# Kernel tuning notes

Measured on AMD Instinct MI355X. Metric: run time of the kernel, lower is better.

## Reference

```python
import jax, jax.numpy as jnp
import numpy as np

DIM = 1024
NUM_HEADS = 16
HEAD_DIM = DIM // NUM_HEADS
SCALE = HEAD_DIM ** -0.5


def setup_inputs() -> dict:
    key = jax.random.key(0)
    ks = jax.random.split(key, 8)
    B, N, L = 2, 256, 8192
    x = jax.random.normal(ks[0], (B, N, DIM), dtype=jnp.float32)
    past_k = jax.random.normal(ks[1], (B, NUM_HEADS, L, HEAD_DIM), dtype=jnp.float32)
    past_v = jax.random.normal(ks[2], (B, NUM_HEADS, L, HEAD_DIM), dtype=jnp.float32)
    s = DIM ** -0.5
    w_qkv = jax.random.normal(ks[3], (DIM, 3 * DIM), dtype=jnp.float32) * s
    b_qkv = jnp.zeros((3 * DIM,), dtype=jnp.float32)
    w_proj = jax.random.normal(ks[4], (DIM, DIM), dtype=jnp.float32) * s
    b_proj = jnp.zeros((DIM,), dtype=jnp.float32)
    return {"x": x, "past_k": past_k, "past_v": past_v,
            "w_qkv": w_qkv, "b_qkv": b_qkv, "w_proj": w_proj, "b_proj": b_proj}


def reference(x, past_k, past_v, w_qkv, b_qkv, w_proj, b_proj):
    B, N, C = x.shape
    qkv = (x @ w_qkv + b_qkv).reshape(B, N, 3, NUM_HEADS, HEAD_DIM)
    qkv = jnp.transpose(qkv, (2, 0, 3, 1, 4))
    q, k_new, v_new = qkv[0], qkv[1], qkv[2]
    # Streaming KV cache append (torch.cat along seq dim)
    k_all = jnp.concatenate([past_k, k_new], axis=-2)  # [B, H, L+N, D]
    v_all = jnp.concatenate([past_v, v_new], axis=-2)
    # Scaled dot-product attention (non-causal full attention over cache)
    scores = jnp.einsum("bhnd,bhld->bhnl", q, k_all) * SCALE
    attn = jax.nn.softmax(scores, axis=-1)
    out = jnp.einsum("bhnl,bhld->bhnd", attn, v_all)  # [B, H, N, D]
    out = jnp.transpose(out, (0, 2, 1, 3)).reshape(B, N, C)
    return out @ w_proj + b_proj
```

## Files before the change

kernel.cpp:

```cpp
#include <hip/hip_runtime.h>
#include <hip/hip_bf16.h>


#define BB 2
#define NH 16
#define NQ 256
#define HD 64
#define DIMC 1024
#define LPAST 8192
#define TOTK 8448
#define NSPLIT 16

typedef __attribute__((ext_vector_type(8))) short short8;
typedef __attribute__((ext_vector_type(4))) float f32x4;
typedef __attribute__((ext_vector_type(16))) float f32x16;
typedef __attribute__((ext_vector_type(4))) int int4v;

#define DEVI static __device__ __forceinline__

DEVI float exp2g(float x) { return __builtin_amdgcn_exp2f(x); }

DEVI int cvtpk(float lo, float hi) {
  int r;
  asm("v_cvt_pk_bf16_f32 %0, %1, %2" : "=v"(r) : "v"(lo), "v"(hi));
  return r;
}
DEVI short f2bf(float f) {
  union { float f; unsigned u; } v; v.f = f;
  unsigned r = v.u + 0x7FFFu + ((v.u >> 16) & 1u);
  return (short)(r >> 16);
}
DEVI void ldsbar() {
  asm volatile("s_waitcnt lgkmcnt(0)" ::: "memory");
  __builtin_amdgcn_s_barrier();
}

template<int MODE>
__global__ __launch_bounds__(256, 2) void gemm_k(
    const float* __restrict__ A, const float* __restrict__ Bm,
    const float* __restrict__ bias, float* __restrict__ Cout,
    short* __restrict__ qbuf, float* __restrict__ knew, float* __restrict__ vnew,
    int M, int Nn, int K)
{
  __shared__ alignas(16) short As[64][72];
  __shared__ alignas(16) short Bs[64][72];
  const int tid = threadIdx.x;
  const int lane = tid & 63, wave = tid >> 6;
  const int nblk = Nn >> 6;
  const int bi = blockIdx.x / nblk, bj = blockIdx.x % nblk;
  const int wm = wave >> 1, wn = wave & 1;
  const int g = lane >> 4, l16 = lane & 15;
  f32x4 acc[2][2] = {};
  const int r = tid >> 2, q4 = (tid & 3) << 4;

  for (int k0 = 0; k0 < K; k0 += 64) {
    const float* pa = A + (size_t)(bi * 64 + r) * K + (k0 + q4);
    float4 a0 = ((const float4*)pa)[0];
    float4 a1 = ((const float4*)pa)[1];
    float4 a2 = ((const float4*)pa)[2];
    float4 a3 = ((const float4*)pa)[3];
    const float* pb = Bm + (size_t)(k0 + r) * Nn + (bj * 64 + q4);
    float4 b0 = ((const float4*)pb)[0];
    float4 b1 = ((const float4*)pb)[1];
    float4 b2 = ((const float4*)pb)[2];
    float4 b3 = ((const float4*)pb)[3];
    ldsbar();
    {
      int4v p0 = {cvtpk(a0.x,a0.y), cvtpk(a0.z,a0.w), cvtpk(a1.x,a1.y), cvtpk(a1.z,a1.w)};
      int4v p1 = {cvtpk(a2.x,a2.y), cvtpk(a2.z,a2.w), cvtpk(a3.x,a3.y), cvtpk(a3.z,a3.w)};
      *(int4v*)&As[r][q4]     = p0;
      *(int4v*)&As[r][q4 + 8] = p1;
    }
    Bs[q4+ 0][r] = f2bf(b0.x); Bs[q4+ 1][r] = f2bf(b0.y);
    Bs[q4+ 2][r] = f2bf(b0.z); Bs[q4+ 3][r] = f2bf(b0.w);
    Bs[q4+ 4][r] = f2bf(b1.x); Bs[q4+ 5][r] = f2bf(b1.y);
    Bs[q4+ 6][r] = f2bf(b1.z); Bs[q4+ 7][r] = f2bf(b1.w);
    Bs[q4+ 8][r] = f2bf(b2.x); Bs[q4+ 9][r] = f2bf(b2.y);
    Bs[q4+10][r] = f2bf(b2.z); Bs[q4+11][r] = f2bf(b2.w);
    Bs[q4+12][r] = f2bf(b3.x); Bs[q4+13][r] = f2bf(b3.y);
    Bs[q4+14][r] = f2bf(b3.z); Bs[q4+15][r] = f2bf(b3.w);
    ldsbar();
    #pragma unroll
    for (int kf = 0; kf < 2; ++kf) {
      short8 af[2], bfv[2];
      #pragma unroll
      for (int mt = 0; mt < 2; ++mt)
        af[mt] = *(const short8*)&As[wm*32 + mt*16 + l16][kf*32 + g*8];
      #pragma unroll
      for (int nt = 0; nt < 2; ++nt)
        bfv[nt] = *(const short8*)&Bs[wn*32 + nt*16 + l16][kf*32 + g*8];
      #pragma unroll
      for (int mt = 0; mt < 2; ++mt)
        #pragma unroll
        for (int nt = 0; nt < 2; ++nt)
          acc[mt][nt] = __builtin_amdgcn_mfma_f32_16x16x32_bf16(
              af[mt], bfv[nt], acc[mt][nt], 0, 0, 0);
    }
  }

  #pragma unroll
  for (int mt = 0; mt < 2; ++mt)
    #pragma unroll
    for (int nt = 0; nt < 2; ++nt)
      #pragma unroll
      for (int rg = 0; rg < 4; ++rg) {
        int row = bi*64 + wm*32 + mt*16 + g*4 + rg;
        int col = bj*64 + wn*32 + nt*16 + l16;
        float val = acc[mt][nt][rg] + bias[col];
        if (MODE == 0) {
          Cout[(size_t)row * Nn + col] = val;
        } else {
          int which = col >> 10, cc = col & 1023;
          int h = cc >> 6, d = cc & 63;
          int b = row >> 8, n = row & 255;
          size_t idx = (((size_t)(b*NH + h))*NQ + n)*HD + d;
          if (which == 0)      qbuf[idx] = f2bf(val * 0.180336878f);
          else if (which == 1) knew[idx] = val;
          else                 vnew[idx] = val;
        }
      }
}

__global__ __launch_bounds__(256, 2) void attn_k(
    const short* __restrict__ qbuf, const float* __restrict__ pastk,
    const float* __restrict__ pastv, const float* __restrict__ knew,
    const float* __restrict__ vnew, _Float16* __restrict__ opart,
    float* __restrict__ mbuf, float* __restrict__ lbuf)
{
  __shared__ alignas(16) short Kt[2][64][64];
  __shared__ alignas(16) short Vt[3][64][64];
  const int tid = threadIdx.x;
  const int lane = tid & 63, qg = tid >> 6;
  const int h = lane >> 5, c = lane & 31;
  const int s = blockIdx.x & (NSPLIT - 1), bh = blockIdx.x / NSPLIT;
  const int kr = tid >> 2, kd16 = (tid & 3) << 4;
  const int vq2 = tid & 31, dg = tid >> 5;
  const int key0 = 2 * vq2;
  const int vpi = ((key0>>5)<<5) | (((key0>>3)&1)<<4) | (((key0>>2)&1)<<3)
                | (((key0>>4)&1)<<2) | (key0&3);
  const int csw = (c & 7) << 3;

  short8 qfA[4], qfB[4];
  #pragma unroll
  for (int dk = 0; dk < 4; ++dk) {
    qfA[dk] = *(const short8*)(qbuf + ((size_t)bh*NQ + qg*64 + c)*HD + 16*dk + 8*h);
    qfB[dk] = *(const short8*)(qbuf + ((size_t)bh*NQ + qg*64 + 32 + c)*HD + 16*dk + 8*h);
  }

  f32x16 accA[2] = {}, accB[2] = {};
  float mA = -INFINITY, lA = 0.f, mB = -INFINITY, lB = 0.f;
  short8 paA[4], paB[4];

  const int first  = 8*s + (s < 4 ? s : 4);
  const int nsteps = 8 + (s < 4 ? 1 : 0);

  float kst[16], vAr[8], vBr[8];
  auto load = [&](int step) {
    const float* kp = (step < 128)
        ? pastk + ((size_t)bh*LPAST + step*64 + kr)*HD + kd16
        : knew  + ((size_t)bh*NQ + (step - 128)*64 + kr)*HD + kd16;
    *(float4*)&kst[0]  = ((const float4*)kp)[0];
    *(float4*)&kst[4]  = ((const float4*)kp)[1];
    *(float4*)&kst[8]  = ((const float4*)kp)[2];
    *(float4*)&kst[12] = ((const float4*)kp)[3];
    const float* vq = (step < 128)
        ? pastv + ((size_t)bh*LPAST + step*64 + key0)*HD + 8*dg
        : vnew  + ((size_t)bh*NQ + (step - 128)*64 + key0)*HD + 8*dg;
    *(float4*)&vAr[0] = ((const float4*)vq)[0];
    *(float4*)&vAr[4] = ((const float4*)vq)[1];
    *(float4*)&vBr[0] = ((const float4*)(vq + HD))[0];
    *(float4*)&vBr[4] = ((const float4*)(vq + HD))[1];
  };
  auto stage_for = [&](int it2) {
    int kb = it2 & 1, vb = it2 % 3;
    int4v k0 = {cvtpk(kst[0],kst[1]),  cvtpk(kst[2],kst[3]),
                cvtpk(kst[4],kst[5]),  cvtpk(kst[6],kst[7])};
    int4v k1 = {cvtpk(kst[8],kst[9]),  cvtpk(kst[10],kst[11]),
                cvtpk(kst[12],kst[13]), cvtpk(kst[14],kst[15])};
    *(int4v*)&Kt[kb][kr][kd16 ^ ((kr & 7) << 3)]       = k0;
    *(int4v*)&Kt[kb][kr][(kd16 + 8) ^ ((kr & 7) << 3)] = k1;
    #pragma unroll
    for (int i = 0; i < 8; ++i) {
      int row = 8*dg + i;
      *(int*)&Vt[vb][row][vpi ^ (i << 3)] = cvtpk(vAr[i], vBr[i]);
    }
  };

  load(first);
  stage_for(0);
  if (nsteps > 1) load(first + 1);
  ldsbar();

  for (int it = 0; it < nsteps; ++it) {
    const int kb = it & 1;

    f32x16 svA0 = {}, svA1 = {}, svB0 = {}, svB1 = {};
    __builtin_amdgcn_s_setprio(1);
    if (it > 0) {
      const int pvb = (it - 1) % 3;
      #pragma unroll
      for (int kc = 0; kc < 4; ++kc) {
        #pragma unroll
        for (int dt = 0; dt < 2; ++dt) {
          short8 vf = *(const short8*)&Vt[pvb][32*dt + c][(16*kc + 8*h) ^ csw];
          accA[dt] = __builtin_amdgcn_mfma_f32_32x32x16_bf16(paA[kc], vf, accA[dt], 0,0,0);
          accB[dt] = __builtin_amdgcn_mfma_f32_32x32x16_bf16(paB[kc], vf, accB[dt], 0,0,0);
        }
      }
    }
    #pragma unroll
    for (int dk = 0; dk < 4; ++dk) {
      short8 k0 = *(const short8*)&Kt[kb][c][(16*dk + 8*h) ^ csw];
      svA0 = __builtin_amdgcn_mfma_f32_32x32x16_bf16(k0, qfA[dk], svA0, 0,0,0);
      svB0 = __builtin_amdgcn_mfma_f32_32x32x16_bf16(k0, qfB[dk], svB0, 0,0,0);
    }
    #pragma unroll
    for (int dk = 0; dk < 4; ++dk) {
      short8 k1 = *(const short8*)&Kt[kb][32 + c][(16*dk + 8*h) ^ csw];
      svA1 = __builtin_amdgcn_mfma_f32_32x32x16_bf16(k1, qfA[dk], svA1, 0,0,0);
      svB1 = __builtin_amdgcn_mfma_f32_32x32x16_bf16(k1, qfB[dk], svB1, 0,0,0);
    }
    __builtin_amdgcn_s_setprio(0);

    if (it + 1 < nsteps) {
      stage_for(it + 1);
      if (it + 2 < nsteps) load(first + it + 2);
    }

    {
      float t16[16];
      #pragma unroll
      for (int r = 0; r < 16; ++r) t16[r] = fmaxf(svA0[r], svA1[r]);
      #pragma unroll
      for (int w = 8; w >= 1; w >>= 1)
        #pragma unroll
        for (int r = 0; r < w; ++r) t16[r] = fmaxf(t16[r], t16[r + w]);
      if (!__all(t16[0] <= mA + 8.f)) {
        float mx = fmaxf(t16[0], __shfl_xor(t16[0], 32));
        float mn = fmaxf(mA, mx);
        float al = exp2g(mA - mn);
        lA *= al;
        #pragma unroll
        for (int r = 0; r < 16; ++r) {
          float a = __shfl(al, (r&3) + 8*(r>>2) + 4*h);
          accA[0][r] *= a; accA[1][r] *= a;
        }
        mA = mn;
      }
      float ss = 0.f;
      #pragma unroll
      for (int r = 0; r < 16; ++r) {
        float p0 = exp2g(svA0[r] - mA); svA0[r] = p0;
        float p1 = exp2g(svA1[r] - mA); svA1[r] = p1;
        ss += p0 + p1;
      }
      lA += ss;
      #pragma unroll
      for (int kc = 0; kc < 4; ++kc) {
        int4v w;
        #pragma unroll
        for (int jd = 0; jd < 4; ++jd) {
          int r0 = 8*(jd>>1) + 4*(kc&1) + 2*(jd&1);
          w[jd] = (kc < 2) ? cvtpk(svA0[r0], svA0[r0+1])
                           : cvtpk(svA1[r0], svA1[r0+1]);
        }
        paA[kc] = __builtin_bit_cast(short8, w);
      }
    }
    {
      float t16[16];
      #pragma unroll
      for (int r = 0; r < 16; ++r) t16[r] = fmaxf(svB0[r], svB1[r]);
      #pragma unroll
      for (int w = 8; w >= 1; w >>= 1)
        #pragma unroll
        for (int r = 0; r < w; ++r) t16[r] = fmaxf(t16[r], t16[r + w]);
      if (!__all(t16[0] <= mB + 8.f)) {
        float mx = fmaxf(t16[0], __shfl_xor(t16[0], 32));
        float mn = fmaxf(mB, mx);
        float al = exp2g(mB - mn);
        lB *= al;
        #pragma unroll
        for (int r = 0; r < 16; ++r) {
          float a = __shfl(al, (r&3) + 8*(r>>2) + 4*h);
          accB[0][r] *= a; accB[1][r] *= a;
        }
        mB = mn;
      }
      float ss = 0.f;
      #pragma unroll
      for (int r = 0; r < 16; ++r) {
        float p0 = exp2g(svB0[r] - mB); svB0[r] = p0;
        float p1 = exp2g(svB1[r] - mB); svB1[r] = p1;
        ss += p0 + p1;
      }
      lB += ss;
      #pragma unroll
      for (int kc = 0; kc < 4; ++kc) {
        int4v w;
        #pragma unroll
        for (int jd = 0; jd < 4; ++jd) {
          int r0 = 8*(jd>>1) + 4*(kc&1) + 2*(jd&1);
          w[jd] = (kc < 2) ? cvtpk(svB0[r0], svB0[r0+1])
                           : cvtpk(svB1[r0], svB1[r0+1]);
        }
        paB[kc] = __builtin_bit_cast(short8, w);
      }
    }

    if (it + 1 < nsteps) ldsbar();
  }

  {
    const int pvb = (nsteps - 1) % 3;
    #pragma unroll
    for (int kc = 0; kc < 4; ++kc) {
      #pragma unroll
      for (int dt = 0; dt < 2; ++dt) {
        short8 vf = *(const short8*)&Vt[pvb][32*dt + c][(16*kc + 8*h) ^ csw];
        accA[dt] = __builtin_amdgcn_mfma_f32_32x32x16_bf16(paA[kc], vf, accA[dt], 0,0,0);
        accB[dt] = __builtin_amdgcn_mfma_f32_32x32x16_bf16(paB[kc], vf, accB[dt], 0,0,0);
      }
    }
  }

  float lAt = lA + __shfl_xor(lA, 32);
  float lBt = lB + __shfl_xor(lB, 32);
  float rA = 1.0f / lAt, rB = 1.0f / lBt;
  size_t pbase = ((size_t)(bh * NSPLIT + s)) * NQ;
  #pragma unroll
  for (int r = 0; r < 16; ++r) {
    int rr = (r&3) + 8*(r>>2) + 4*h;
    float rAr = __shfl(rA, rr);
    float rBr = __shfl(rB, rr);
    #pragma unroll
    for (int dt = 0; dt < 2; ++dt) {
      opart[(pbase + qg*64 + rr)*HD + 32*dt + c]      = (_Float16)(accA[dt][r] * rAr);
      opart[(pbase + qg*64 + 32 + rr)*HD + 32*dt + c] = (_Float16)(accB[dt][r] * rBr);
    }
  }
  if (lane < 32) {
    mbuf[pbase + qg*64 + c]      = mA;
    lbuf[pbase + qg*64 + c]      = lAt;
    mbuf[pbase + qg*64 + 32 + c] = mB;
    lbuf[pbase + qg*64 + 32 + c] = lBt;
  }
}

__global__ __launch_bounds__(256) void combine_k(
    const _Float16* __restrict__ opart, const float* __restrict__ mbuf,
    const float* __restrict__ lbuf, float* __restrict__ attnout)
{
  const int lane = threadIdx.x & 63, wave = threadIdx.x >> 6;
  const int rid = blockIdx.x * 4 + wave;
  const int bh = rid >> 8, n = rid & 255;
  const int b = bh >> 4, h = bh & 15;
  float M = -INFINITY;
  float ms[NSPLIT], ls[NSPLIT];
  #pragma unroll
  for (int s = 0; s < NSPLIT; ++s) {
    size_t base = ((size_t)(bh * NSPLIT + s)) * NQ + n;
    ms[s] = mbuf[base]; ls[s] = lbuf[base];
    M = fmaxf(M, ms[s]);
  }
  float denom = 0.f, o = 0.f;
  #pragma unroll
  for (int s = 0; s < NSPLIT; ++s) {
    float w = exp2g(ms[s] - M) * ls[s];
    denom += w;
    o += w * (float)opart[(((size_t)(bh * NSPLIT + s)) * NQ + n) * HD + lane];
  }
  attnout[((size_t)(b * NQ + n)) * DIMC + h * HD + lane] = o / denom;
}

extern "C" void kernel_launch(void* const* d_in, const int* in_sizes, int n_in,
                              void* d_out, int out_size, void* d_ws, size_t ws_size,
                              hipStream_t stream)
{
  const float* x     = (const float*)d_in[0];
  const float* pastk = (const float*)d_in[1];
  const float* pastv = (const float*)d_in[2];
  const float* wqkv  = (const float*)d_in[3];
  const float* bqkv  = (const float*)d_in[4];
  const float* wproj = (const float*)d_in[5];
  const float* bproj = (const float*)d_in[6];
  float* out = (float*)d_out;
  char* ws = (char*)d_ws;

  size_t off = 0;
  short* qbuf     = (short*)(ws + off);     off += (size_t)BB*NH*NQ*HD*2;
  float* knew     = (float*)(ws + off);     off += (size_t)BB*NH*NQ*HD*4;
  float* vnew     = (float*)(ws + off);     off += (size_t)BB*NH*NQ*HD*4;
  _Float16* opart = (_Float16*)(ws + off);  off += (size_t)BB*NH*NSPLIT*NQ*HD*2;
  float* mbuf     = (float*)(ws + off);     off += (size_t)BB*NH*NSPLIT*NQ*4;
  float* lbuf     = (float*)(ws + off);     off += (size_t)BB*NH*NSPLIT*NQ*4;
  float* attnout  = (float*)(ws + off);     off += (size_t)BB*NQ*DIMC*4;

  gemm_k<1><<<(512/64)*(3072/64), 256, 0, stream>>>(
      x, wqkv, bqkv, nullptr, qbuf, knew, vnew, 512, 3072, 1024);
  attn_k<<<BB*NH*NSPLIT, 256, 0, stream>>>(
      qbuf, pastk, pastv, knew, vnew, opart, mbuf, lbuf);
  combine_k<<<BB*NH*NQ/4, 256, 0, stream>>>(opart, mbuf, lbuf, attnout);
  gemm_k<0><<<(512/64)*(1024/64), 256, 0, stream>>>(
      attnout, wproj, bproj, out, nullptr, nullptr, nullptr, 512, 1024, 1024);
}
```

Baseline: 84.53 us.

## Raise attention split count and occupancy, serialize QK halves to cut registers

Increases the KV split count from 16 to 24 and raises the launch bound to 3 blocks per CU, so more blocks are resident at once. To fit that register budget, the B-half score MFMAs now run after the A-half softmax instead of together with it, which shrinks the live score accumulators. The V load/staging pattern changes to four keys per thread with int2 LDS writes, and the split ranges are rebalanced for 132 steps over 24 splits. The cost is more partial results to merge and less overlap between the two query halves within a wave.

```diff
diff --git a/kernel.cpp b/kernel.cpp
--- a/kernel.cpp
+++ b/kernel.cpp
@@ -9,7 +9,7 @@
 #define DIMC 1024
 #define LPAST 8192
 #define TOTK 8448
-#define NSPLIT 16
+#define NSPLIT 24
 
 typedef __attribute__((ext_vector_type(8))) short short8;
 typedef __attribute__((ext_vector_type(4))) float f32x4;
@@ -121,7 +121,7 @@
       }
 }
 
-__global__ __launch_bounds__(256, 2) void attn_k(
+__global__ __launch_bounds__(256, 3) void attn_k(
     const short* __restrict__ qbuf, const float* __restrict__ pastk,
     const float* __restrict__ pastv, const float* __restrict__ knew,
     const float* __restrict__ vnew, _Float16* __restrict__ opart,
@@ -132,12 +132,12 @@
   const int tid = threadIdx.x;
   const int lane = tid & 63, qg = tid >> 6;
   const int h = lane >> 5, c = lane & 31;
-  const int s = blockIdx.x & (NSPLIT - 1), bh = blockIdx.x / NSPLIT;
+  const int s = blockIdx.x % NSPLIT, bh = blockIdx.x / NSPLIT;
   const int kr = tid >> 2, kd16 = (tid & 3) << 4;
-  const int vq2 = tid & 31, dg = tid >> 5;
-  const int key0 = 2 * vq2;
+  const int vq4 = tid & 15, dgg = tid >> 4;
+  const int key0 = 4 * vq4;
   const int vpi = ((key0>>5)<<5) | (((key0>>3)&1)<<4) | (((key0>>2)&1)<<3)
-                | (((key0>>4)&1)<<2) | (key0&3);
+                | (((key0>>4)&1)<<2);
   const int csw = (c & 7) << 3;
 
   short8 qfA[4], qfB[4];
@@ -151,10 +151,11 @@
   float mA = -INFINITY, lA = 0.f, mB = -INFINITY, lB = 0.f;
   short8 paA[4], paB[4];
 
-  const int first  = 8*s + (s < 4 ? s : 4);
-  const int nsteps = 8 + (s < 4 ? 1 : 0);
-
-  float kst[16], vAr[8], vBr[8];
+  const int first  = (s < 12) ? 6*s : 5*s + 12;
+  const int nsteps = (s < 12) ? 6 : 5;
+
+  float kst[16];
+  float4 vk0, vk1, vk2, vk3;
   auto load = [&](int step) {
     const float* kp = (step < 128)
         ? pastk + ((size_t)bh*LPAST + step*64 + kr)*HD + kd16
@@ -164,12 +165,12 @@
     *(float4*)&kst[8]  = ((const float4*)kp)[2];
     *(float4*)&kst[12] = ((const float4*)kp)[3];
     const float* vq = (step < 128)
-        ? pastv + ((size_t)bh*LPAST + step*64 + key0)*HD + 8*dg
-        : vnew  + ((size_t)bh*NQ + (step - 128)*64 + key0)*HD + 8*dg;
-    *(float4*)&vAr[0] = ((const float4*)vq)[0];
-    *(float4*)&vAr[4] = ((const float4*)vq)[1];
-    *(float4*)&vBr[0] = ((const float4*)(vq + HD))[0];
-    *(float4*)&vBr[4] = ((const float4*)(vq + HD))[1];
+        ? pastv + ((size_t)bh*LPAST + step*64 + key0)*HD + 4*dgg
+        : vnew  + ((size_t)bh*NQ + (step - 128)*64 + key0)*HD + 4*dgg;
+    vk0 = *(const float4*)(vq);
+    vk1 = *(const float4*)(vq + HD);
+    vk2 = *(const float4*)(vq + 2*HD);
+    vk3 = *(const float4*)(vq + 3*HD);
   };
   auto stage_for = [&](int it2) {
     int kb = it2 & 1, vb = it2 % 3;
@@ -179,10 +180,15 @@
                 cvtpk(kst[12],kst[13]), cvtpk(kst[14],kst[15])};
     *(int4v*)&Kt[kb][kr][kd16 ^ ((kr & 7) << 3)]       = k0;
     *(int4v*)&Kt[kb][kr][(kd16 + 8) ^ ((kr & 7) << 3)] = k1;
-    #pragma unroll
-    for (int i = 0; i < 8; ++i) {
-      int row = 8*dg + i;
-      *(int*)&Vt[vb][row][vpi ^ (i << 3)] = cvtpk(vAr[i], vBr[i]);
+    const float* f0 = (const float*)&vk0;
+    const float* f1 = (const float*)&vk1;
+    const float* f2 = (const float*)&vk2;
+    const float* f3 = (const float*)&vk3;
+    #pragma unroll
+    for (int i = 0; i < 4; ++i) {
+      int row = 4*dgg + i;
+      int2 w = make_int2(cvtpk(f0[i], f1[i]), cvtpk(f2[i], f3[i]));
+      *(int2*)&Vt[vb][row][vpi ^ ((row & 7) << 3)] = w;
     }
   };
 
@@ -194,7 +200,7 @@
   for (int it = 0; it < nsteps; ++it) {
     const int kb = it & 1;
 
-    f32x16 svA0 = {}, svA1 = {}, svB0 = {}, svB1 = {};
+    f32x16 svA0 = {}, svA1 = {};
     __builtin_amdgcn_s_setprio(1);
     if (it > 0) {
       const int pvb = (it - 1) % 3;
@@ -211,21 +217,11 @@
     #pragma unroll
     for (int dk = 0; dk < 4; ++dk) {
       short8 k0 = *(const short8*)&Kt[kb][c][(16*dk + 8*h) ^ csw];
+      short8 k1 = *(const short8*)&Kt[kb][32 + c][(16*dk + 8*h) ^ csw];
       svA0 = __builtin_amdgcn_mfma_f32_32x32x16_bf16(k0, qfA[dk], svA0, 0,0,0);
-      svB0 = __builtin_amdgcn_mfma_f32_32x32x16_bf16(k0, qfB[dk], svB0, 0,0,0);
-    }
-    #pragma unroll
-    for (int dk = 0; dk < 4; ++dk) {
-      short8 k1 = *(const short8*)&Kt[kb][32 + c][(16*dk + 8*h) ^ csw];
       svA1 = __builtin_amdgcn_mfma_f32_32x32x16_bf16(k1, qfA[dk], svA1, 0,0,0);
-      svB1 = __builtin_amdgcn_mfma_f32_32x32x16_bf16(k1, qfB[dk], svB1, 0,0,0);
     }
     __builtin_amdgcn_s_setprio(0);
-
-    if (it + 1 < nsteps) {
-      stage_for(it + 1);
-      if (it + 2 < nsteps) load(first + it + 2);
-    }
 
     {
       float t16[16];
@@ -267,6 +263,23 @@
         paA[kc] = __builtin_bit_cast(short8, w);
       }
     }
+
+    f32x16 svB0 = {}, svB1 = {};
+    __builtin_amdgcn_s_setprio(1);
+    #pragma unroll
+    for (int dk = 0; dk < 4; ++dk) {
+      short8 k0 = *(const short8*)&Kt[kb][c][(16*dk + 8*h) ^ csw];
+      short8 k1 = *(const short8*)&Kt[kb][32 + c][(16*dk + 8*h) ^ csw];
+      svB0 = __builtin_amdgcn_mfma_f32_32x32x16_bf16(k0, qfB[dk], svB0, 0,0,0);
+      svB1 = __builtin_amdgcn_mfma_f32_32x32x16_bf16(k1, qfB[dk], svB1, 0,0,0);
+    }
+    __builtin_amdgcn_s_setprio(0);
+
+    if (it + 1 < nsteps) {
+      stage_for(it + 1);
+      if (it + 2 < nsteps) load(first + it + 2);
+    }
+
     {
       float t16[16];
       #pragma unroll
```

New measurement: 179.9 us. +112.8%, slower.
